# Optimization experiments

Measured on AMD Instinct MI355X. Metric: run time of the kernel, lower is better.

The kernel has to match this reference:

```python
import jax, jax.numpy as jnp
import numpy as np

B, I, O, H = 32768, 16, 16, 512  # batch, in_dim, out_dim, hid_dim
NEG_SLOPE = 0.2


def setup_inputs() -> dict:
    key = jax.random.key(0)
    k_x, k_w1, k_b1, k_w2, k_b2 = jax.random.split(key, 5)
    x = jax.random.normal(k_x, (B, I), dtype=jnp.float32)

    # Per-output first-layer weights, init like the torch module:
    # randn, small |w|<0.01 replaced by +-0.01, then masked by jacobian_support row.
    support = jnp.ones((O, I), dtype=jnp.float32)  # jacobian_support (all ones)
    W1 = jax.random.normal(k_w1, (O, H, I), dtype=jnp.float32)
    adjusted = 0.02 * (W1 >= 0).astype(jnp.float32) - 0.01
    W1 = jnp.where(jnp.abs(W1) < 0.01, adjusted, W1) * support[:, None, :]

    # Biases / second layer: torch default Linear init, uniform(-1/sqrt(fan_in), 1/sqrt(fan_in))
    bnd1 = 1.0 / np.sqrt(I)
    bnd2 = 1.0 / np.sqrt(H)
    b1 = jax.random.uniform(k_b1, (O, H), dtype=jnp.float32, minval=-bnd1, maxval=bnd1)
    W2 = jax.random.uniform(k_w2, (O, H), dtype=jnp.float32, minval=-bnd2, maxval=bnd2)
    b2 = jax.random.uniform(k_b2, (O,), dtype=jnp.float32, minval=-bnd2, maxval=bnd2)
    return {"x": x, "W1": W1, "b1": b1, "W2": W2, "b2": b2}


def reference(x, W1, b1, W2, b2):
    # Fused batched GEMM over all out_dim heads (replaces the python loop).
    # hidden: [B, O, H]
    h = jnp.einsum('bi,ohi->boh', x, W1) + b1
    h = jnp.where(h >= 0, h, NEG_SLOPE * h)  # LeakyReLU(0.2)
    # second layer maps H -> 1 per head; concatenated output: [B, O]
    out = jnp.einsum('boh,oh->bo', h, W2) + b2
    return out
```

## Files before the change

kernel.cpp:

```cpp
#include <hip/hip_runtime.h>


#define B_DIM 32768
#define I_DIM 16
#define O_DIM 16
#define H_DIM 512

typedef _Float16 f16x4 __attribute__((ext_vector_type(4)));
typedef _Float16 f16x8 __attribute__((ext_vector_type(8)));
typedef __fp16   h16x2 __attribute__((ext_vector_type(2)));
typedef float    f32x4 __attribute__((ext_vector_type(4)));
typedef int      i32x2 __attribute__((ext_vector_type(2)));
typedef int      i32x4 __attribute__((ext_vector_type(4)));

__global__ __launch_bounds__(512, 2) void mlp_fused(
    const float* __restrict__ x, const float* __restrict__ W1,
    const float* __restrict__ b1, const float* __restrict__ W2,
    const float* __restrict__ b2, float* __restrict__ out) {
    __shared__ f16x8 sm_a1[1024];
    __shared__ f16x8 sm_w2[1024];
    __shared__ float sm_b1[512];
    __shared__ float red[512];
    __shared__ float v_sm[16];
    __shared__ float c_sm;

    const int tid = threadIdx.x;
    const int o   = blockIdx.x & 15;
    const int grp = blockIdx.x >> 4;
    const float* W1o = W1 + (size_t)o * H_DIM * I_DIM;
    const float* W2o = W2 + (size_t)o * H_DIM;
    const float* b1o = b1 + (size_t)o * H_DIM;

#pragma unroll
    for (int i = 0; i < 2; ++i) {
        const int e = tid + 512 * i;
        const int l = e & 63, p = e >> 6;
        const int row = l & 15, kg = l >> 4;
        const float* a_base = W1o + ((size_t)(2 * p * 16 + row) * I_DIM + kg * 4);
        const f32x4 a0 = *reinterpret_cast<const f32x4*>(a_base);
        const f32x4 a1v = *reinterpret_cast<const f32x4*>(a_base + 16 * I_DIM);
        f16x8 va;
#pragma unroll
        for (int j = 0; j < 4; ++j) { va[j] = (_Float16)a0[j]; va[4 + j] = (_Float16)a1v[j]; }
        sm_a1[e] = va;
        const float* w_base = W2o + p * 32 + kg * 4;
        const f32x4 w0 = *reinterpret_cast<const f32x4*>(w_base);
        const f32x4 w1v = *reinterpret_cast<const f32x4*>(w_base + 16);
        f16x8 vw;
#pragma unroll
        for (int j = 0; j < 4; ++j) {
            vw[j]     = (_Float16)(0.4f * w0[j]);
            vw[4 + j] = (_Float16)(0.4f * w1v[j]);
        }
        sm_w2[e] = vw;
    }
    sm_b1[tid] = b1o[tid];

    {
        const int i = tid & 15, hc = tid >> 4;
        float acc = 0.f;
#pragma unroll
        for (int hh = 0; hh < 16; ++hh) {
            const int h = hc * 16 + hh;
            acc = fmaf(W2o[h], W1o[(size_t)h * I_DIM + i], acc);
        }
        red[tid] = acc;
    }
    __syncthreads();
    if (tid < 16) {
        float s = 0.f;
#pragma unroll
        for (int k = 0; k < 32; ++k) s += red[tid + 16 * k];
        v_sm[tid] = 0.6f * s;
    }
    float cpart = W2o[tid] * b1o[tid];
    __syncthreads();
    red[tid] = cpart;
    __syncthreads();
    if (tid < 64) {
        float s = 0.f;
#pragma unroll
        for (int k = 0; k < 8; ++k) s += red[tid + 64 * k];
#pragma unroll
        for (int m = 1; m <= 32; m <<= 1) s += __shfl_xor(s, m, 64);
        if (tid == 0) c_sm = 0.6f * s + b2[o];
    }
    __syncthreads();

    const int lane = tid & 63, w = tid >> 6;
    const int col = lane & 15, kg = lane >> 4;

    for (int half = 0; half < 2; ++half) {
        const int tile0 = grp * 128 + half * 64 + w * 8;

        f16x4 xf[8];
#pragma unroll
        for (int t = 0; t < 8; ++t) {
            const f32x4 xv = *reinterpret_cast<const f32x4*>(
                x + (size_t)((tile0 + t) * 16 + col) * I_DIM + kg * 4);
            h16x2 q0 = __builtin_amdgcn_cvt_pkrtz(xv[0], xv[1]);
            h16x2 q1 = __builtin_amdgcn_cvt_pkrtz(xv[2], xv[3]);
            i32x2 xi; xi[0] = __builtin_bit_cast(int, q0); xi[1] = __builtin_bit_cast(int, q1);
            xf[t] = __builtin_bit_cast(f16x4, xi);
        }

        f16x4 vlf;
#pragma unroll
        for (int j = 0; j < 4; ++j) vlf[j] = (_Float16)v_sm[kg * 4 + j];
        const float c0 = c_sm;
        const f32x4 linC = {c0, c0, c0, c0};

        f32x4 acc[8];
#pragma unroll
        for (int t = 0; t < 8; ++t)
            acc[t] = __builtin_amdgcn_mfma_f32_16x16x16f16(xf[t], vlf, linC, 0, 0, 0);

#pragma unroll 2
        for (int p = 0; p < 16; ++p) {
            const f16x8 a1pair = sm_a1[p * 64 + lane];
            const f16x4 A1a = __builtin_shufflevector(a1pair, a1pair, 0, 1, 2, 3);
            const f16x4 A1b = __builtin_shufflevector(a1pair, a1pair, 4, 5, 6, 7);
            const f16x8 W2f = sm_w2[p * 64 + lane];
            const f32x4 bC0 = *reinterpret_cast<const f32x4*>(&sm_b1[p * 32 + kg * 4]);
            const f32x4 bC1 = *reinterpret_cast<const f32x4*>(&sm_b1[p * 32 + 16 + kg * 4]);
#pragma unroll
            for (int t = 0; t < 8; ++t) {
                f32x4 d0 = __builtin_amdgcn_mfma_f32_16x16x16f16(A1a, xf[t], bC0, 0, 0, 0);
                f32x4 d1 = __builtin_amdgcn_mfma_f32_16x16x16f16(A1b, xf[t], bC1, 0, 0, 0);
                h16x2 p0 = __builtin_amdgcn_cvt_pkrtz(fabsf(d0[0]), fabsf(d0[1]));
                h16x2 p1 = __builtin_amdgcn_cvt_pkrtz(fabsf(d0[2]), fabsf(d0[3]));
                h16x2 p2 = __builtin_amdgcn_cvt_pkrtz(fabsf(d1[0]), fabsf(d1[1]));
                h16x2 p3 = __builtin_amdgcn_cvt_pkrtz(fabsf(d1[2]), fabsf(d1[3]));
                i32x4 ai;
                ai[0] = __builtin_bit_cast(int, p0); ai[1] = __builtin_bit_cast(int, p1);
                ai[2] = __builtin_bit_cast(int, p2); ai[3] = __builtin_bit_cast(int, p3);
                f16x8 A2 = __builtin_bit_cast(f16x8, ai);
                acc[t] = __builtin_amdgcn_mfma_f32_16x16x32_f16(A2, W2f, acc[t], 0, 0, 0);
            }
        }

        if (col < 4) {
#pragma unroll
            for (int t = 0; t < 8; ++t) {
                float v = (col == 0) ? acc[t][0] : (col == 1) ? acc[t][1]
                        : (col == 2) ? acc[t][2] : acc[t][3];
                out[(size_t)((tile0 + t) * 16 + kg * 4 + col) * O_DIM + o] = v;
            }
        }
    }
}

extern "C" void kernel_launch(void* const* d_in, const int* in_sizes, int n_in,
                              void* d_out, int out_size, void* d_ws, size_t ws_size,
                              hipStream_t stream) {
    const float* x  = (const float*)d_in[0];
    const float* W1 = (const float*)d_in[1];
    const float* b1 = (const float*)d_in[2];
    const float* W2 = (const float*)d_in[3];
    const float* b2 = (const float*)d_in[4];
    float* out = (float*)d_out;

    mlp_fused<<<256, 512, 0, stream>>>(x, W1, b1, W2, b2, out);
}
```

Measured before the change: 26.54 us.

## Fuse prologue reductions into weight staging and prefetch first x tile

Computes the W2·W1 linear-term partial sums while staging W1/W2 into shared memory instead of re-reading W1 in a separate loop. Merges the two prologue reductions into one pass, cutting the barrier count from four to two. Issues the first half's x loads before the barrier so their latency overlaps the reduction. Adds an 8KB shared-memory buffer, which may affect occupancy at two blocks per CU.

```diff
diff --git a/kernel.cpp b/kernel.cpp
--- a/kernel.cpp
+++ b/kernel.cpp
@@ -20,6 +20,7 @@
     __shared__ f16x8 sm_a1[1024];
     __shared__ f16x8 sm_w2[1024];
     __shared__ float sm_b1[512];
+    __shared__ f32x4 red4[512];
     __shared__ float red[512];
     __shared__ float v_sm[16];
     __shared__ float c_sm;
@@ -31,19 +32,28 @@
     const float* W2o = W2 + (size_t)o * H_DIM;
     const float* b1o = b1 + (size_t)o * H_DIM;
 
+    const int lane = tid & 63, w = tid >> 6;
+    const int col = lane & 15, kg = lane >> 4;
+
+    f32x4 vpart = {0.f, 0.f, 0.f, 0.f};
 #pragma unroll
     for (int i = 0; i < 2; ++i) {
         const int e = tid + 512 * i;
         const int l = e & 63, p = e >> 6;
-        const int row = l & 15, kg = l >> 4;
-        const float* a_base = W1o + ((size_t)(2 * p * 16 + row) * I_DIM + kg * 4);
+        const int row = l & 15, kgs = l >> 4;
+        const float* a_base = W1o + ((size_t)(2 * p * 16 + row) * I_DIM + kgs * 4);
         const f32x4 a0 = *reinterpret_cast<const f32x4*>(a_base);
         const f32x4 a1v = *reinterpret_cast<const f32x4*>(a_base + 16 * I_DIM);
         f16x8 va;
 #pragma unroll
         for (int j = 0; j < 4; ++j) { va[j] = (_Float16)a0[j]; va[4 + j] = (_Float16)a1v[j]; }
         sm_a1[e] = va;
-        const float* w_base = W2o + p * 32 + kg * 4;
+        const float w2a = W2o[2 * p * 16 + row];
+        const float w2b = W2o[2 * p * 16 + 16 + row];
+#pragma unroll
+        for (int j = 0; j < 4; ++j)
+            vpart[j] = fmaf(w2b, a1v[j], fmaf(w2a, a0[j], vpart[j]));
+        const float* w_base = W2o + p * 32 + kgs * 4;
         const f32x4 w0 = *reinterpret_cast<const f32x4*>(w_base);
         const f32x4 w1v = *reinterpret_cast<const f32x4*>(w_base + 16);
         f16x8 vw;
@@ -54,46 +64,16 @@
         }
         sm_w2[e] = vw;
     }
-    sm_b1[tid] = b1o[tid];
+    {
+        const float b1v = b1o[tid];
+        sm_b1[tid] = b1v;
+        red[tid]   = W2o[tid] * b1v;
+        red4[tid]  = vpart;
+    }
 
+    f16x4 xf0[8];
     {
-        const int i = tid & 15, hc = tid >> 4;
-        float acc = 0.f;
-#pragma unroll
-        for (int hh = 0; hh < 16; ++hh) {
-            const int h = hc * 16 + hh;
-            acc = fmaf(W2o[h], W1o[(size_t)h * I_DIM + i], acc);
-        }
-        red[tid] = acc;
-    }
-    __syncthreads();
-    if (tid < 16) {
-        float s = 0.f;
-#pragma unroll
-        for (int k = 0; k < 32; ++k) s += red[tid + 16 * k];
-        v_sm[tid] = 0.6f * s;
-    }
-    float cpart = W2o[tid] * b1o[tid];
-    __syncthreads();
-    red[tid] = cpart;
-    __syncthreads();
-    if (tid < 64) {
-        float s = 0.f;
-#pragma unroll
-        for (int k = 0; k < 8; ++k) s += red[tid + 64 * k];
-#pragma unroll
-        for (int m = 1; m <= 32; m <<= 1) s += __shfl_xor(s, m, 64);
-        if (tid == 0) c_sm = 0.6f * s + b2[o];
-    }
-    __syncthreads();
-
-    const int lane = tid & 63, w = tid >> 6;
-    const int col = lane & 15, kg = lane >> 4;
-
-    for (int half = 0; half < 2; ++half) {
-        const int tile0 = grp * 128 + half * 64 + w * 8;
-
-        f16x4 xf[8];
+        const int tile0 = grp * 128 + w * 8;
 #pragma unroll
         for (int t = 0; t < 8; ++t) {
             const f32x4 xv = *reinterpret_cast<const f32x4*>(
@@ -101,7 +81,51 @@
             h16x2 q0 = __builtin_amdgcn_cvt_pkrtz(xv[0], xv[1]);
             h16x2 q1 = __builtin_amdgcn_cvt_pkrtz(xv[2], xv[3]);
             i32x2 xi; xi[0] = __builtin_bit_cast(int, q0); xi[1] = __builtin_bit_cast(int, q1);
-            xf[t] = __builtin_bit_cast(f16x4, xi);
+            xf0[t] = __builtin_bit_cast(f16x4, xi);
+        }
+    }
+    __syncthreads();
+
+    if (tid < 64) {
+        f32x4 s = red4[tid];
+#pragma unroll
+        for (int k = 1; k < 8; ++k) s += red4[tid + 64 * k];
+#pragma unroll
+        for (int m = 1; m <= 8; m <<= 1) {
+#pragma unroll
+            for (int c = 0; c < 4; ++c) s[c] += __shfl_xor(s[c], m, 64);
+        }
+        if ((tid & 15) == 0) {
+            const int kgw = tid >> 4;
+#pragma unroll
+            for (int j = 0; j < 4; ++j) v_sm[kgw * 4 + j] = 0.6f * s[j];
+        }
+        float cs = 0.f;
+#pragma unroll
+        for (int k = 0; k < 8; ++k) cs += red[tid + 64 * k];
+#pragma unroll
+        for (int m = 1; m <= 32; m <<= 1) cs += __shfl_xor(cs, m, 64);
+        if (tid == 0) c_sm = 0.6f * cs + b2[o];
+    }
+    __syncthreads();
+
+    for (int half = 0; half < 2; ++half) {
+        const int tile0 = grp * 128 + half * 64 + w * 8;
+
+        f16x4 xf[8];
+        if (half == 0) {
+#pragma unroll
+            for (int t = 0; t < 8; ++t) xf[t] = xf0[t];
+        } else {
+#pragma unroll
+            for (int t = 0; t < 8; ++t) {
+                const f32x4 xv = *reinterpret_cast<const f32x4*>(
+                    x + (size_t)((tile0 + t) * 16 + col) * I_DIM + kg * 4);
+                h16x2 q0 = __builtin_amdgcn_cvt_pkrtz(xv[0], xv[1]);
+                h16x2 q1 = __builtin_amdgcn_cvt_pkrtz(xv[2], xv[3]);
+                i32x2 xi; xi[0] = __builtin_bit_cast(int, q0); xi[1] = __builtin_bit_cast(int, q1);
+                xf[t] = __builtin_bit_cast(f16x4, xi);
+            }
         }
 
         f16x4 vlf;
```

Result: no change. 26.32 us (median of 2 runs) (-0.8%).
